# Performance work log

Measured on AMD Instinct MI355X. Metric: run time of the kernel, lower is better.

Reference implementation:

```python
import jax, jax.numpy as jnp
import numpy as np

B, SQ, SKV = 4, 4096, 1024
QDIM, CDIM = 1024, 768
HEADS, DHEAD = 16, 64
INNER = HEADS * DHEAD


def setup_inputs() -> dict:
    key = jax.random.key(0)
    ks = jax.random.split(key, 7)
    s = 0.02
    return {
        "x": jax.random.normal(ks[0], (B, SQ, QDIM), dtype=jnp.float32),
        "context": jax.random.normal(ks[1], (B, SKV, CDIM), dtype=jnp.float32),
        "Wq": jax.random.normal(ks[2], (QDIM, INNER), dtype=jnp.float32) * s,
        "Wk": jax.random.normal(ks[3], (CDIM, INNER), dtype=jnp.float32) * s,
        "Wv": jax.random.normal(ks[4], (CDIM, INNER), dtype=jnp.float32) * s,
        "Wo": jax.random.normal(ks[5], (INNER, QDIM), dtype=jnp.float32) * s,
        "bo": jnp.zeros((QDIM,), dtype=jnp.float32),
    }


def reference(x, context, Wq, Wk, Wv, Wo, bo):
    # QKV projections (no bias, matching bias=False Linear layers)
    q = x @ Wq          # [B, SQ, INNER]
    k = context @ Wk    # [B, SKV, INNER]
    v = context @ Wv    # [B, SKV, INNER]

    # split heads: b s (h d) -> b h s d
    def split_heads(t, s):
        return t.reshape(B, s, HEADS, DHEAD).transpose(0, 2, 1, 3)

    qh = split_heads(q, SQ)
    kh = split_heads(k, SKV)
    vh = split_heads(v, SKV)

    scale = DHEAD ** -0.5  # attention_basic default scale
    sim = jnp.einsum('bhqd,bhkd->bhqk', qh, kh) * scale  # [B,H,SQ,SKV]
    attn = jax.nn.softmax(sim, axis=-1)
    out = jnp.einsum('bhqk,bhkd->bhqd', attn, vh)        # [B,H,SQ,DHEAD]
    out = out.transpose(0, 2, 1, 3).reshape(B, SQ, INNER)

    # output projection (Linear with bias); dropout p=0 -> identity
    return out @ Wo + bo
```

## Files before the change

### kernel.cpp

```cpp
#include <hip/hip_runtime.h>


typedef unsigned short u16;
typedef unsigned int u32;
typedef __bf16 bf16x8 __attribute__((ext_vector_type(8)));
typedef float float4v __attribute__((ext_vector_type(4)));
typedef _Float16 half4 __attribute__((ext_vector_type(4)));
typedef _Float16 half8 __attribute__((ext_vector_type(8)));
typedef _Float16 half2v __attribute__((ext_vector_type(2)));
typedef u32 u32x2 __attribute__((ext_vector_type(2)));
typedef u32 u32x4 __attribute__((ext_vector_type(4)));
typedef __attribute__((address_space(1))) void as1_void;
typedef __attribute__((address_space(3))) void as3_void;

__device__ __forceinline__ u16 f2bf(float f) {
  unsigned u = __float_as_uint(f);
  u += 0x7FFF + ((u >> 16) & 1);
  return (u16)(u >> 16);
}

__device__ __forceinline__ void async16(const u16* g, u16* l) {
  __builtin_amdgcn_global_load_lds((as1_void*)(void*)g, (as3_void*)l, 16, 0, 0);
}

#define WAITCNT_VM8 0xF78
#define WAITCNT_VM4 0xF74
#define WAITCNT_VM0 0xF70

__global__ void cvt_kernel(const float* __restrict__ x, u16* __restrict__ xbf,
                           const float* __restrict__ ctx, u16* __restrict__ ctxbf) {
  int i = blockIdx.x * 256 + threadIdx.x;
  const float* in; u16* out; int j;
  if (i < 4194304) { in = x; out = xbf; j = i; }
  else if (i < 4980736) { in = ctx; out = ctxbf; j = i - 4194304; }
  else return;
  float4 v = ((const float4*)in)[j];
  ushort4 o;
  o.x = f2bf(v.x); o.y = f2bf(v.y); o.z = f2bf(v.z); o.w = f2bf(v.w);
  ((ushort4*)out)[j] = o;
}

__global__ void twt_kernel(const float* __restrict__ Wq, const float* __restrict__ Wk,
                           const float* __restrict__ Wv, const float* __restrict__ Wo,
                           u16* __restrict__ WqT, u16* __restrict__ WkT,
                           u16* __restrict__ WvT, u16* __restrict__ WoT) {
  __shared__ u16 t[32][33];
  int z = blockIdx.z;
  const float* W = z == 0 ? Wq : z == 1 ? Wk : z == 2 ? Wv : Wo;
  u16* Wt = z == 0 ? WqT : z == 1 ? WkT : z == 2 ? WvT : WoT;
  int Kd = (z == 1 || z == 2) ? 768 : 1024;
  int k0 = blockIdx.y * 32;
  if (k0 >= Kd) return;
  int tx = threadIdx.x, ty = threadIdx.y;
  int n0 = blockIdx.x * 32;
#pragma unroll
  for (int i = 0; i < 4; i++)
    t[ty + i * 8][tx] = f2bf(W[(size_t)(k0 + ty + i * 8) * 1024 + n0 + tx]);
  __syncthreads();
#pragma unroll
  for (int i = 0; i < 4; i++)
    Wt[(size_t)(n0 + ty + i * 8) * Kd + k0 + tx] = t[tx][ty + i * 8];
}


__device__ __forceinline__ void ld_a4(const u16 (*Lp)[256][8], int rbase, int quad,
                                      int l15, bf16x8 a[4][2]) {
#pragma unroll
  for (int mi = 0; mi < 4; mi++)
#pragma unroll
    for (int ks = 0; ks < 2; ks++)
      a[mi][ks] = *(const bf16x8*)&Lp[ks * 4 + quad][rbase + mi * 16 + l15][0];
}

__device__ __forceinline__ void ld_b2(const u16 (*Lp)[256][8], int rbase, int quad,
                                      int l15, bf16x8 b[2][2]) {
#pragma unroll
  for (int ni = 0; ni < 2; ni++)
#pragma unroll
    for (int ks = 0; ks < 2; ks++)
      b[ni][ks] = *(const bf16x8*)&Lp[ks * 4 + quad][rbase + ni * 16 + l15][0];
}

__device__ __forceinline__ void mm16(bf16x8 a[4][2], bf16x8 b[2][2],
                                     float4v acc[8][4], int mh, int nh) {
  __builtin_amdgcn_s_setprio(1);
#pragma unroll
  for (int mi = 0; mi < 4; mi++)
#pragma unroll
    for (int ni = 0; ni < 2; ni++)
#pragma unroll
      for (int ks = 0; ks < 2; ks++)
        acc[mh * 4 + mi][nh * 2 + ni] = __builtin_amdgcn_mfma_f32_16x16x32_bf16(
            a[mi][ks], b[ni][ks], acc[mh * 4 + mi][nh * 2 + ni], 0, 0, 0);
  __builtin_amdgcn_s_setprio(0);
}

__device__ __forceinline__ void gemm256_core(const u16* __restrict__ A,
                                             const u16* __restrict__ Bt, int K,
                                             int m0, int n0, float4v acc[8][4]) {
  __shared__ __align__(16) u16 L[2][2][8][256][8];
  int tid = threadIdx.x;
  int w = tid >> 6, lane = tid & 63;
  int l15 = lane & 15, quad = lane >> 4;
  int wm = (w >> 2) * 128, wn = (w & 3) * 64;

  int c0 = 2 * w, c1 = 2 * w + 1;
  int kc0 = c0 & 7, mb0 = (c0 >> 3) * 64;
  int kc1 = c1 & 7, mb1 = (c1 >> 3) * 64;
  const u16* pA0 = A + (size_t)(m0 + mb0 + lane) * K + kc0 * 8;
  const u16* pA1 = A + (size_t)(m0 + mb1 + lane) * K + kc1 * 8;
  const u16* pB0 = Bt + (size_t)(n0 + mb0 + lane) * K + kc0 * 8;
  const u16* pB1 = Bt + (size_t)(n0 + mb1 + lane) * K + kc1 * 8;
  size_t hs = (size_t)128 * K;

#define STG_A(buf, t)                                                          \
  do {                                                                         \
    const u16* s0 = pA0 + (size_t)(t) * 64;                                    \
    const u16* s1 = pA1 + (size_t)(t) * 64;                                    \
    async16(s0, &L[buf][0][kc0][mb0][0]);                                      \
    async16(s1, &L[buf][0][kc1][mb1][0]);                                      \
    async16(s0 + hs, &L[buf][0][kc0][128 + mb0][0]);                           \
    async16(s1 + hs, &L[buf][0][kc1][128 + mb1][0]);                           \
  } while (0)
#define STG_B(buf, t)                                                          \
  do {                                                                         \
    const u16* s0 = pB0 + (size_t)(t) * 64;                                    \
    const u16* s1 = pB1 + (size_t)(t) * 64;                                    \
    async16(s0, &L[buf][1][kc0][mb0][0]);                                      \
    async16(s1, &L[buf][1][kc1][mb1][0]);                                      \
    async16(s0 + hs, &L[buf][1][kc0][128 + mb0][0]);                           \
    async16(s1 + hs, &L[buf][1][kc1][128 + mb1][0]);                           \
  } while (0)

  STG_A(0, 0); STG_B(0, 0);
  STG_A(1, 1); STG_B(1, 1);
  __builtin_amdgcn_s_waitcnt(WAITCNT_VM8);
  __builtin_amdgcn_s_barrier();

  bf16x8 a[4][2], b0[2][2], b1[2][2];
  int I = K >> 7;
  for (int i = 0; i < I; ++i) {
    int st = (i + 1 < I);
    ld_a4(L[0][0], wm, quad, l15, a);
    ld_b2(L[0][1], wn, quad, l15, b0);
    if (i > 0) STG_B(1, 2 * i + 1);
    __builtin_amdgcn_s_barrier();
    mm16(a, b0, acc, 0, 0);
    __builtin_amdgcn_s_barrier();
    ld_b2(L[0][1], wn + 32, quad, l15, b1);
    __builtin_amdgcn_s_barrier();
    mm16(a, b1, acc, 0, 1);
    __builtin_amdgcn_s_barrier();
    ld_a4(L[0][0], wm + 64, quad, l15, a);
    __builtin_amdgcn_s_barrier();
    mm16(a, b1, acc, 1, 1);
    __builtin_amdgcn_s_barrier();
    if (st) STG_A(0, 2 * i + 2);
    __builtin_amdgcn_s_barrier();
    mm16(a, b0, acc, 1, 0);
    if (st) __builtin_amdgcn_s_waitcnt(WAITCNT_VM4);
    else    __builtin_amdgcn_s_waitcnt(WAITCNT_VM0);
    __builtin_amdgcn_s_barrier();
    ld_a4(L[1][0], wm, quad, l15, a);
    ld_b2(L[1][1], wn, quad, l15, b0);
    if (st) STG_B(0, 2 * i + 2);
    __builtin_amdgcn_s_barrier();
    mm16(a, b0, acc, 0, 0);
    __builtin_amdgcn_s_barrier();
    ld_b2(L[1][1], wn + 32, quad, l15, b1);
    __builtin_amdgcn_s_barrier();
    mm16(a, b1, acc, 0, 1);
    __builtin_amdgcn_s_barrier();
    ld_a4(L[1][0], wm + 64, quad, l15, a);
    __builtin_amdgcn_s_barrier();
    mm16(a, b1, acc, 1, 1);
    __builtin_amdgcn_s_barrier();
    if (st) STG_A(1, 2 * i + 3);
    __builtin_amdgcn_s_barrier();
    mm16(a, b0, acc, 1, 0);
    if (st) __builtin_amdgcn_s_waitcnt(WAITCNT_VM4);
    __builtin_amdgcn_s_barrier();
  }
#undef STG_A
#undef STG_B
}

__global__ __launch_bounds__(512, 2) void qkv_gemm8(
    const u16* __restrict__ xbf, const u16* __restrict__ ctxbf,
    const u16* __restrict__ WqT, const u16* __restrict__ WkT, const u16* __restrict__ WvT,
    u16* __restrict__ Qb, u16* __restrict__ Kbuf, u16* __restrict__ Vtb, float qscale) {
  int bx = blockIdx.x;
  const u16* A; const u16* Bt; u16* C; int K, mode, m0, n0; float scale;
  if (bx < 256)      { int t = bx;       A = xbf;   Bt = WqT; C = Qb;   K = 1024; mode = 0; scale = qscale; m0 = (t >> 2) * 256; n0 = (t & 3) * 256; }
  else if (bx < 320) { int t = bx - 256; A = ctxbf; Bt = WkT; C = Kbuf; K = 768;  mode = 0; scale = 1.0f;   m0 = (t >> 2) * 256; n0 = (t & 3) * 256; }
  else               { int t = bx - 320; A = ctxbf; Bt = WvT; C = Vtb;  K = 768;  mode = 2; scale = 1.0f;   m0 = (t >> 2) * 256; n0 = (t & 3) * 256; }

  float4v acc[8][4] = {};
  gemm256_core(A, Bt, K, m0, n0, acc);

  int tid = threadIdx.x;
  int w = tid >> 6, lane = tid & 63;
  int l15 = lane & 15, quad = lane >> 4;
  int wm = (w >> 2) * 128, wn = (w & 3) * 64;

  if (mode == 0) {
#pragma unroll
    for (int mi = 0; mi < 8; mi++) {
      int rowb = m0 + wm + mi * 16 + quad * 4;
#pragma unroll
      for (int ni = 0; ni < 4; ni++) {
        int col = n0 + wn + ni * 16 + l15;
#pragma unroll
        for (int r = 0; r < 4; r++)
          C[(size_t)(rowb + r) * 1024 + col] = f2bf(acc[mi][ni][r] * scale);
      }
    }
  } else {
#pragma unroll
    for (int mi = 0; mi < 8; mi++) {
      int rowb = m0 + wm + mi * 16 + quad * 4;
#pragma unroll
      for (int ni = 0; ni < 4; ni++) {
        int col = n0 + wn + ni * 16 + l15;
        int hh = col >> 6, dd = col & 63;
#pragma unroll
        for (int r = 0; r < 4; r++) {
          int rr = rowb + r;
          int b = rr >> 10, skv = rr & 1023;
          _Float16 hv = (_Float16)acc[mi][ni][r];
          C[((((size_t)b * 16 + hh) * 64 + dd) << 10) + skv] = __builtin_bit_cast(u16, hv);
        }
      }
    }
  }
}

__global__ __launch_bounds__(512, 2) void gemm_bt8(
    const u16* __restrict__ A, const u16* __restrict__ Bt,
    float* __restrict__ C, const float* __restrict__ bias) {
  int bx = blockIdx.x;
  int m0 = (bx >> 2) * 256, n0 = (bx & 3) * 256;

  float4v acc[8][4] = {};
  gemm256_core(A, Bt, 1024, m0, n0, acc);

  int tid = threadIdx.x;
  int w = tid >> 6, lane = tid & 63;
  int l15 = lane & 15, quad = lane >> 4;
  int wm = (w >> 2) * 128, wn = (w & 3) * 64;

#pragma unroll
  for (int mi = 0; mi < 8; mi++) {
    int rowb = m0 + wm + mi * 16 + quad * 4;
#pragma unroll
    for (int ni = 0; ni < 4; ni++) {
      int col = n0 + wn + ni * 16 + l15;
      float bv = bias[col];
#pragma unroll
      for (int r = 0; r < 4; r++)
        C[(size_t)(rowb + r) * 1024 + col] = acc[mi][ni][r] + bv;
    }
  }
}

__global__ __launch_bounds__(512, 4) void attn_kernel(
    const u16* __restrict__ Q, const u16* __restrict__ Kb,
    const u16* __restrict__ Vt, u16* __restrict__ Oout) {
  __shared__ __align__(16) u16 lK[2][4096];
  __shared__ __align__(16) u16 lV[2][4096];
  int tid = threadIdx.x, w = tid >> 6, lane = tid & 63;
  int l15 = lane & 15, quad = lane >> 4;
  int bh = blockIdx.y, b = bh >> 4, h = bh & 15;
  int q0 = blockIdx.x * 256 + w * 32;

  const u16* Qbase = Q + ((size_t)(b * 4096 + q0)) * 1024 + h * 64;
  const u16* Kbase = Kb + ((size_t)b << 20) + h * 64;
  const u16* Vbase = Vt + ((size_t)bh << 16);

  bf16x8 qf[2][2];
#pragma unroll
  for (int qt = 0; qt < 2; qt++)
#pragma unroll
    for (int c = 0; c < 2; c++)
      qf[qt][c] = *(const bf16x8*)(Qbase + (size_t)(qt * 16 + l15) * 1024 + c * 32 + quad * 8);

  int x0 = ((tid & 7) ^ ((tid >> 3) & 7)) * 8, r0 = (tid >> 3) * 1024;
  const u16* ks0 = Kbase + r0 + x0;
  const u16* vs0 = Vbase + r0 + x0;
  int kdo0 = w * 512;

  async16(ks0, &lK[0][kdo0]);
  async16(vs0, &lV[0][kdo0]);
  ks0 += 65536;
  vs0 += 64;

  float4v o[2][4] = {};
  float4v osum[2] = {};
  const half8 ones8 = {(_Float16)1.0f, (_Float16)1.0f, (_Float16)1.0f, (_Float16)1.0f,
                       (_Float16)1.0f, (_Float16)1.0f, (_Float16)1.0f, (_Float16)1.0f};

  int lb = l15 & 7;
  int xk0 = ((0 + quad) ^ lb) * 16 + l15 * 128;
  int xk1 = ((4 + quad) ^ lb) * 16 + l15 * 128;
  int vrow = l15 * 128;
  int idx_lo = (((quad & 1) << 5) + l15) << 2;
  int idx_hi = idx_lo + 64;
  bool useb = (quad & 2) != 0;

  for (int it = 0; it < 16; ++it) {
    const char* bK = (const char*)lK + (it & 1) * 8192;
    const char* bV = (const char*)lV + (it & 1) * 8192;
    __syncthreads();
    if (it < 15) {
      int nb = (it + 1) & 1;
      async16(ks0, &lK[nb][kdo0]);
      async16(vs0, &lV[nb][kdo0]);
      ks0 += 65536;
      vs0 += 64;
    }
#pragma unroll
    for (int s = 0; s < 2; ++s) {
      half4 pp[2][2];
#pragma unroll
      for (int hp = 0; hp < 2; ++hp) {
        int sub = s * 2 + hp;
        const char* kb = bK + sub * 2048;
        float4v sv[2] = {{0.f, 0.f, 0.f, 0.f}, {0.f, 0.f, 0.f, 0.f}};
        __builtin_amdgcn_s_setprio(1);
#pragma unroll
        for (int c = 0; c < 2; c++) {
          bf16x8 kf = *(const bf16x8*)(kb + (c ? xk1 : xk0));
#pragma unroll
          for (int qt = 0; qt < 2; qt++)
            sv[qt] = __builtin_amdgcn_mfma_f32_16x16x32_bf16(kf, qf[qt][c], sv[qt], 0, 0, 0);
        }
        __builtin_amdgcn_s_setprio(0);
#pragma unroll
        for (int qt = 0; qt < 2; qt++) {
          float e0 = exp2f(sv[qt][0]), e1 = exp2f(sv[qt][1]);
          float e2 = exp2f(sv[qt][2]), e3 = exp2f(sv[qt][3]);
          half2v p01 = __builtin_bit_cast(half2v, __builtin_amdgcn_cvt_pkrtz(e0, e1));
          half2v p23 = __builtin_bit_cast(half2v, __builtin_amdgcn_cvt_pkrtz(e2, e3));
          pp[hp][qt] = __builtin_shufflevector(p01, p23, 0, 1, 2, 3);
        }
      }
      half8 p8s[2];
#pragma unroll
      for (int qt = 0; qt < 2; qt++) {
        u32x2 a2 = __builtin_bit_cast(u32x2, pp[0][qt]);
        u32x2 b2 = __builtin_bit_cast(u32x2, pp[1][qt]);
        int al0 = __builtin_amdgcn_ds_bpermute(idx_lo, (int)a2[0]);
        int ah0 = __builtin_amdgcn_ds_bpermute(idx_lo, (int)a2[1]);
        int al1 = __builtin_amdgcn_ds_bpermute(idx_hi, (int)a2[0]);
        int ah1 = __builtin_amdgcn_ds_bpermute(idx_hi, (int)a2[1]);
        int bl0 = __builtin_amdgcn_ds_bpermute(idx_lo, (int)b2[0]);
        int bh0 = __builtin_amdgcn_ds_bpermute(idx_lo, (int)b2[1]);
        int bl1 = __builtin_amdgcn_ds_bpermute(idx_hi, (int)b2[0]);
        int bh1 = __builtin_amdgcn_ds_bpermute(idx_hi, (int)b2[1]);
        u32x4 od;
        od[0] = (u32)(useb ? bl0 : al0);
        od[1] = (u32)(useb ? bh0 : ah0);
        od[2] = (u32)(useb ? bl1 : al1);
        od[3] = (u32)(useb ? bh1 : ah1);
        half8 p8 = __builtin_bit_cast(half8, od);
        p8s[qt] = p8;
        osum[qt] = __builtin_amdgcn_mfma_f32_16x16x32_f16(ones8, p8, osum[qt], 0, 0, 0);
      }
      __builtin_amdgcn_s_setprio(1);
#pragma unroll
      for (int dt = 0; dt < 4; dt++) {
        half8 vf = *(const half8*)(bV + dt * 2048 + vrow + (((s * 4 + quad) ^ lb) * 16));
#pragma unroll
        for (int qt = 0; qt < 2; qt++)
          o[qt][dt] = __builtin_amdgcn_mfma_f32_16x16x32_f16(vf, p8s[qt], o[qt][dt], 0, 0, 0);
      }
      __builtin_amdgcn_s_setprio(0);
    }
  }

#pragma unroll
  for (int qt = 0; qt < 2; qt++) {
    float inv = 1.0f / osum[qt][0];
    u16* Ob = Oout + ((size_t)(b * 4096 + q0 + qt * 16 + l15)) * 1024 + h * 64 + quad * 4;
#pragma unroll
    for (int dt = 0; dt < 4; dt++) {
      ushort4 pk;
      pk.x = f2bf(o[qt][dt][0] * inv);
      pk.y = f2bf(o[qt][dt][1] * inv);
      pk.z = f2bf(o[qt][dt][2] * inv);
      pk.w = f2bf(o[qt][dt][3] * inv);
      *(ushort4*)(Ob + dt * 16) = pk;
    }
  }
}

extern "C" void kernel_launch(void* const* d_in, const int* in_sizes, int n_in,
                              void* d_out, int out_size, void* d_ws, size_t ws_size,
                              hipStream_t stream) {
  const float* x   = (const float*)d_in[0];
  const float* ctx = (const float*)d_in[1];
  const float* Wq  = (const float*)d_in[2];
  const float* Wk  = (const float*)d_in[3];
  const float* Wv  = (const float*)d_in[4];
  const float* Wo  = (const float*)d_in[5];
  const float* bo  = (const float*)d_in[6];
  float* out = (float*)d_out;

  u16* ws    = (u16*)d_ws;
  u16* xbf   = ws;
  u16* ctxbf = xbf + 16777216;
  u16* WqT   = ctxbf + 3145728;
  u16* WkT   = WqT + 1048576;
  u16* WvT   = WkT + 786432;
  u16* WoT   = WvT + 786432;
  u16* Qb    = WoT + 1048576;
  u16* Kbuf  = Qb + 16777216;
  u16* Vtb   = Kbuf + 4194304;
  if (ws_size < (size_t)48758784 * 2) return;

  cvt_kernel<<<19456, 256, 0, stream>>>(x, xbf, ctx, ctxbf);
  twt_kernel<<<dim3(32, 32, 4), dim3(32, 8), 0, stream>>>(Wq, Wk, Wv, Wo, WqT, WkT, WvT, WoT);
  qkv_gemm8<<<dim3(384), dim3(512), 0, stream>>>(xbf, ctxbf, WqT, WkT, WvT,
                                                 Qb, Kbuf, Vtb, 0.18033688011112042f);
  attn_kernel<<<dim3(16, 64), dim3(512), 0, stream>>>(Qb, Kbuf, Vtb, xbf);
  gemm_bt8<<<dim3(256), dim3(512), 0, stream>>>(xbf, WoT, out, bo);
}
```

Before: 390.8 us.

## Load K/V fragments directly from global memory in attention, dropping LDS staging

The attention kernel no longer stages K and V tiles in double-buffered shared memory via async global-to-LDS loads with barriers. Each wave now reads its MFMA K and V operands straight from global memory, relying on L2/L1 caching for reuse across waves. The block size is halved to 256 threads with twice as many blocks. This removes the LDS traffic and per-iteration __syncthreads, but each wave now issues its own global loads, so K/V reuse depends on the cache and load latency is no longer hidden by prefetch.

```diff
diff --git a/kernel.cpp b/kernel.cpp
--- a/kernel.cpp
+++ b/kernel.cpp
@@ -263,19 +263,17 @@
   }
 }
 
-__global__ __launch_bounds__(512, 4) void attn_kernel(
+__global__ __launch_bounds__(256, 4) void attn_kernel(
     const u16* __restrict__ Q, const u16* __restrict__ Kb,
     const u16* __restrict__ Vt, u16* __restrict__ Oout) {
-  __shared__ __align__(16) u16 lK[2][4096];
-  __shared__ __align__(16) u16 lV[2][4096];
   int tid = threadIdx.x, w = tid >> 6, lane = tid & 63;
   int l15 = lane & 15, quad = lane >> 4;
   int bh = blockIdx.y, b = bh >> 4, h = bh & 15;
-  int q0 = blockIdx.x * 256 + w * 32;
+  int q0 = blockIdx.x * 128 + w * 32;
 
   const u16* Qbase = Q + ((size_t)(b * 4096 + q0)) * 1024 + h * 64;
-  const u16* Kbase = Kb + ((size_t)b << 20) + h * 64;
-  const u16* Vbase = Vt + ((size_t)bh << 16);
+  const u16* kp = Kb + ((size_t)b << 20) + h * 64 + (size_t)l15 * 1024 + quad * 8;
+  const u16* vp = Vt + ((size_t)bh << 16) + (size_t)l15 * 1024 + quad * 8;
 
   bf16x8 qf[2][2];
 #pragma unroll
@@ -283,53 +281,31 @@
 #pragma unroll
     for (int c = 0; c < 2; c++)
       qf[qt][c] = *(const bf16x8*)(Qbase + (size_t)(qt * 16 + l15) * 1024 + c * 32 + quad * 8);
-
-  int x0 = ((tid & 7) ^ ((tid >> 3) & 7)) * 8, r0 = (tid >> 3) * 1024;
-  const u16* ks0 = Kbase + r0 + x0;
-  const u16* vs0 = Vbase + r0 + x0;
-  int kdo0 = w * 512;
-
-  async16(ks0, &lK[0][kdo0]);
-  async16(vs0, &lV[0][kdo0]);
-  ks0 += 65536;
-  vs0 += 64;
 
   float4v o[2][4] = {};
   float4v osum[2] = {};
   const half8 ones8 = {(_Float16)1.0f, (_Float16)1.0f, (_Float16)1.0f, (_Float16)1.0f,
                        (_Float16)1.0f, (_Float16)1.0f, (_Float16)1.0f, (_Float16)1.0f};
 
-  int lb = l15 & 7;
-  int xk0 = ((0 + quad) ^ lb) * 16 + l15 * 128;
-  int xk1 = ((4 + quad) ^ lb) * 16 + l15 * 128;
-  int vrow = l15 * 128;
   int idx_lo = (((quad & 1) << 5) + l15) << 2;
   int idx_hi = idx_lo + 64;
   bool useb = (quad & 2) != 0;
 
   for (int it = 0; it < 16; ++it) {
-    const char* bK = (const char*)lK + (it & 1) * 8192;
-    const char* bV = (const char*)lV + (it & 1) * 8192;
-    __syncthreads();
-    if (it < 15) {
-      int nb = (it + 1) & 1;
-      async16(ks0, &lK[nb][kdo0]);
-      async16(vs0, &lV[nb][kdo0]);
-      ks0 += 65536;
-      vs0 += 64;
-    }
+    const u16* kit = kp + (size_t)it * 65536;
+    const u16* vit = vp + it * 64;
 #pragma unroll
     for (int s = 0; s < 2; ++s) {
       half4 pp[2][2];
 #pragma unroll
       for (int hp = 0; hp < 2; ++hp) {
         int sub = s * 2 + hp;
-        const char* kb = bK + sub * 2048;
+        const u16* ks = kit + sub * 16384;
         float4v sv[2] = {{0.f, 0.f, 0.f, 0.f}, {0.f, 0.f, 0.f, 0.f}};
         __builtin_amdgcn_s_setprio(1);
 #pragma unroll
         for (int c = 0; c < 2; c++) {
-          bf16x8 kf = *(const bf16x8*)(kb + (c ? xk1 : xk0));
+          bf16x8 kf = *(const bf16x8*)(ks + c * 32);
 #pragma unroll
           for (int qt = 0; qt < 2; qt++)
             sv[qt] = __builtin_amdgcn_mfma_f32_16x16x32_bf16(kf, qf[qt][c], sv[qt], 0, 0, 0);
@@ -369,7 +345,7 @@
       __builtin_amdgcn_s_setprio(1);
 #pragma unroll
       for (int dt = 0; dt < 4; dt++) {
-        half8 vf = *(const half8*)(bV + dt * 2048 + vrow + (((s * 4 + quad) ^ lb) * 16));
+        half8 vf = *(const half8*)(vit + (size_t)dt * 16384 + s * 32);
 #pragma unroll
         for (int qt = 0; qt < 2; qt++)
           o[qt][dt] = __builtin_amdgcn_mfma_f32_16x16x32_f16(vf, p8s[qt], o[qt][dt], 0, 0, 0);
@@ -422,6 +398,6 @@
   twt_kernel<<<dim3(32, 32, 4), dim3(32, 8), 0, stream>>>(Wq, Wk, Wv, Wo, WqT, WkT, WvT, WoT);
   qkv_gemm8<<<dim3(384), dim3(512), 0, stream>>>(xbf, ctxbf, WqT, WkT, WvT,
                                                  Qb, Kbuf, Vtb, 0.18033688011112042f);
-  attn_kernel<<<dim3(16, 64), dim3(512), 0, stream>>>(Qb, Kbuf, Vtb, xbf);
+  attn_kernel<<<dim3(32, 64), dim3(256), 0, stream>>>(Qb, Kbuf, Vtb, xbf);
   gemm_bt8<<<dim3(256), dim3(512), 0, stream>>>(xbf, WoT, out, bo);
 }
```

Result: slower. 518.7 us (+32.7%).
